# Kernel optimization log

Measured on AMD Instinct MI355X. Metric: run time of the kernel, lower is better.

The kernel has to match this reference:

```python
import jax, jax.numpy as jnp
import numpy as np

B, S, H = 2, 2048, 2048
NH, HD = 32, 64            # num heads, head dim (H = NH*HD)
FFN = 8192
EPS = 1e-5


def _layernorm(x, g, b):
    mu = jnp.mean(x, axis=-1, keepdims=True)
    var = jnp.mean(jnp.square(x - mu), axis=-1, keepdims=True)
    return (x - mu) * jax.lax.rsqrt(var + EPS) * g + b


def setup_inputs() -> dict:
    key = jax.random.key(0)
    ks = jax.random.split(key, 8)
    s = lambda fan_in: 1.0 / np.sqrt(fan_in)
    return {
        "x": jax.random.normal(ks[0], (B, S, H), dtype=jnp.float32),
        "ln1_g": jnp.ones((H,), jnp.float32),
        "ln1_b": jnp.zeros((H,), jnp.float32),
        "w_qkv": jax.random.normal(ks[1], (H, 3 * H), jnp.float32) * s(H),
        "b_qkv": jnp.zeros((3 * H,), jnp.float32),
        "w_proj": jax.random.normal(ks[2], (H, H), jnp.float32) * s(H),
        "b_proj": jnp.zeros((H,), jnp.float32),
        "ln2_g": jnp.ones((H,), jnp.float32),
        "ln2_b": jnp.zeros((H,), jnp.float32),
        "w1": jax.random.normal(ks[3], (H, FFN), jnp.float32) * s(H),
        "b1": jnp.zeros((FFN,), jnp.float32),
        "w2": jax.random.normal(ks[4], (FFN, H), jnp.float32) * s(FFN),
        "b2": jnp.zeros((H,), jnp.float32),
    }


def reference(x, ln1_g, ln1_b, w_qkv, b_qkv, w_proj, b_proj,
              ln2_g, ln2_b, w1, b1, w2, b2):
    # Pre-LN attention block (dropout in eval mode -> identity)
    res = x
    h = _layernorm(x, ln1_g, ln1_b)
    qkv = h @ w_qkv + b_qkv                       # [B,S,3H]
    qkv = qkv.reshape(B, S, NH, 3 * HD)           # matches tf reshape+split on axis 3
    q, k, v = jnp.split(qkv, 3, axis=3)           # each [B,S,NH,HD]
    scores = jnp.einsum('bqhd,bkhd->bhqk', q, k) / jnp.sqrt(jnp.float32(HD))
    probs = jax.nn.softmax(scores, axis=-1)       # [B,NH,S,S]
    ctx = jnp.einsum('bhqk,bkhd->bqhd', probs, v).reshape(B, S, H)
    x = ctx @ w_proj + b_proj
    x = res + x
    # Pre-LN MLP block
    res = x
    h = _layernorm(x, ln2_g, ln2_b)
    h = jax.nn.gelu(h @ w1 + b1, approximate=True)
    h = h @ w2 + b2
    return h + res
```

## Files before the change

### kernel.cpp

```cpp
#include <hip/hip_runtime.h>
#include <hip/hip_bf16.h>
#include <math.h>


typedef __attribute__((ext_vector_type(8))) short bf16x8;
typedef __attribute__((ext_vector_type(4))) float f32x4;
typedef __attribute__((ext_vector_type(16))) float f32x16;

#define DEV __device__ __forceinline__

static constexpr int SEQ  = 2048;
static constexpr int HID  = 2048;
static constexpr int NHEAD = 32;
static constexpr int HDIM = 64;
static constexpr int NFFN = 8192;
static constexpr int NTOK = 2 * SEQ;
static constexpr int QKVW = 3 * HID;

#define QSCALE 0.1803368801111204f

#if defined(__has_builtin)
#if __has_builtin(__builtin_amdgcn_exp2f)
#define EXP2(x) __builtin_amdgcn_exp2f(x)
#endif
#endif
#ifndef EXP2
#define EXP2(x) exp2f(x)
#endif

DEV ushort f2bf(float f) {
  unsigned u = __float_as_uint(f);
  return (ushort)((u + 0x7fffu + ((u >> 16) & 1u)) >> 16);
}

DEV void gload16(const void* g, void* l) {
  __builtin_amdgcn_global_load_lds(
      (const __attribute__((address_space(1))) unsigned int*)g,
      (__attribute__((address_space(3))) unsigned int*)l, 16, 0, 0);
}

__global__ __launch_bounds__(256) void tcvt_kernel(const float* __restrict__ in,
                                                   ushort* __restrict__ out,
                                                   int R, int C) {
  __shared__ ushort tile[64][72];
  const int tr = blockIdx.y * 64, tc = blockIdx.x * 64;
  const int t = threadIdx.x;
  const int rr = t >> 2, c4 = (t & 3) * 16;
  const float4* ip = (const float4*)(in + (size_t)(tr + rr) * C + tc + c4);
  float4 a0 = ip[0], a1 = ip[1], a2 = ip[2], a3 = ip[3];
  ushort* tp = &tile[rr][c4];
  tp[0]=f2bf(a0.x); tp[1]=f2bf(a0.y); tp[2]=f2bf(a0.z); tp[3]=f2bf(a0.w);
  tp[4]=f2bf(a1.x); tp[5]=f2bf(a1.y); tp[6]=f2bf(a1.z); tp[7]=f2bf(a1.w);
  tp[8]=f2bf(a2.x); tp[9]=f2bf(a2.y); tp[10]=f2bf(a2.z); tp[11]=f2bf(a2.w);
  tp[12]=f2bf(a3.x); tp[13]=f2bf(a3.y); tp[14]=f2bf(a3.z); tp[15]=f2bf(a3.w);
  __syncthreads();
  union { ushort u[8]; bf16x8 v; } p0, p1;
#pragma unroll
  for (int j = 0; j < 8; ++j) { p0.u[j] = tile[c4 + j][rr]; p1.u[j] = tile[c4 + 8 + j][rr]; }
  ushort* op = out + (size_t)(tc + rr) * R + tr + c4;
  *(bf16x8*)op = p0.v;
  *(bf16x8*)(op + 8) = p1.v;
}

__global__ __launch_bounds__(256) void ln_kernel(const float* __restrict__ x,
                                                 const float* __restrict__ g,
                                                 const float* __restrict__ bb,
                                                 ushort* __restrict__ out) {
  const int row = blockIdx.x, t = threadIdx.x;
  const float4* xv = (const float4*)(x + (size_t)row * HID);
  float4 a0 = xv[t * 2], a1 = xv[t * 2 + 1];
  float s  = a0.x + a0.y + a0.z + a0.w + a1.x + a1.y + a1.z + a1.w;
  float ss = a0.x*a0.x + a0.y*a0.y + a0.z*a0.z + a0.w*a0.w
           + a1.x*a1.x + a1.y*a1.y + a1.z*a1.z + a1.w*a1.w;
#pragma unroll
  for (int o = 32; o > 0; o >>= 1) { s += __shfl_down(s, o); ss += __shfl_down(ss, o); }
  __shared__ float red[8];
  const int w = t >> 6, l = t & 63;
  if (l == 0) { red[w] = s; red[4 + w] = ss; }
  __syncthreads();
  s  = red[0] + red[1] + red[2] + red[3];
  ss = red[4] + red[5] + red[6] + red[7];
  const float mu = s * (1.f / HID);
  const float rs = rsqrtf(ss * (1.f / HID) - mu * mu + 1e-5f);
  const float4* gv = (const float4*)g;
  const float4* bv = (const float4*)bb;
  float4 g0 = gv[t * 2], g1 = gv[t * 2 + 1], b0 = bv[t * 2], b1 = bv[t * 2 + 1];
  union { ushort u[8]; bf16x8 v; } p;
  p.u[0] = f2bf((a0.x - mu) * rs * g0.x + b0.x);
  p.u[1] = f2bf((a0.y - mu) * rs * g0.y + b0.y);
  p.u[2] = f2bf((a0.z - mu) * rs * g0.z + b0.z);
  p.u[3] = f2bf((a0.w - mu) * rs * g0.w + b0.w);
  p.u[4] = f2bf((a1.x - mu) * rs * g1.x + b1.x);
  p.u[5] = f2bf((a1.y - mu) * rs * g1.y + b1.y);
  p.u[6] = f2bf((a1.z - mu) * rs * g1.z + b1.z);
  p.u[7] = f2bf((a1.w - mu) * rs * g1.w + b1.w);
  *(bf16x8*)(out + (size_t)row * HID + t * 8) = p.v;
}

DEV void qkv_store(int row, int col, float v,
                   ushort* __restrict__ qpk, ushort* __restrict__ kpk,
                   ushort* __restrict__ vpk) {
  const int h = col / 192;
  const int c = col - h * 192;
  const int bh2 = (row >> 11) * 32 + h;
  const int t32 = (row >> 5) & 63;
  const int r5 = row & 31;
  if (c < 64) {
    const int s = c >> 4, hi2 = (c >> 3) & 1, j = c & 7;
    qpk[(((size_t)bh2 * 64 + t32) * 4 + s) * 512 + (hi2 * 32 + r5) * 8 + j] = f2bf(v * QSCALE);
  } else if (c < 128) {
    const int d = c - 64;
    const int s = d >> 4, hi2 = (d >> 3) & 1, j = d & 7;
    kpk[(((size_t)bh2 * 64 + t32) * 4 + s) * 512 + (hi2 * 32 + r5) * 8 + j] = f2bf(v);
  } else {
    const int d = c - 128;
    const int ks = r5 >> 4, hi2 = (r5 >> 3) & 1, j = r5 & 7;
    const int half = d >> 5, dl = d & 31;
    vpk[((((size_t)bh2 * 64 + t32) * 2 + ks) * 2 + half) * 512 + (hi2 * 32 + dl) * 8 + j] = f2bf(v);
  }
}

DEV bf16x8 ldsfrag(const char* base, int row, int slot) {
  return *(const bf16x8*)(base + row * 128 + (((slot ^ (row & 7)) << 4)));
}

DEV void stage_one(const ushort* __restrict__ src, int Kd, int trow, int kt,
                   char* dst, int w, int lr, int lsl, int i) {
  const int g = i * 8 + w;
  gload16(src + (size_t)(trow + g * 8 + lr) * Kd + kt + ((lsl ^ lr) << 3),
          dst + (g * 8 + lr) * 128 + lsl * 16);
}

template <int BM, int EPI>
__global__ __launch_bounds__(512, 2) void gemm8p_kernel(
    const ushort* __restrict__ A, const ushort* __restrict__ BT,
    const float* __restrict__ bias, const float* __restrict__ res,
    void* __restrict__ outv,
    ushort* __restrict__ qpk, ushort* __restrict__ kpk, ushort* __restrict__ vpk,
    int M, int N, int K) {
  constexpr int MR = BM / 32;
  constexpr int MH = MR / 2;
  constexpr int AI = BM / 64;
  constexpr int NI = AI + 4;
  constexpr int SPP = (BM == 256) ? 3 : 2;

  __shared__ ushort lds[2 * (BM * 64 + 256 * 64)];
  char* const a0p = (char*)lds;
  char* const b0p = a0p + BM * 128;
  char* const a1p = b0p + 32768;
  char* const b1p = a1p + BM * 128;

  const int t = threadIdx.x;
  const int w = t >> 6, l = t & 63;
  const int l16 = l & 15, lg = l >> 4;
  const int lr = l >> 3, lsl = l & 7;
  const int wm = w >> 2, wn = w & 3;

  const int nwg = gridDim.x * gridDim.y;
  const int lin = blockIdx.y * gridDim.x + blockIdx.x;
  const int work = (lin & 7) * (nwg >> 3) + (lin >> 3);
  const int bn = work % gridDim.x, bm = work / gridDim.x;
  const int tm = bm * BM, tn = bn * 256;

  const f32x4 z4 = {0.f, 0.f, 0.f, 0.f};
  f32x4 acc[MR][4];
#pragma unroll
  for (int i = 0; i < MR; ++i)
#pragma unroll
    for (int j = 0; j < 4; ++j) acc[i][j] = z4;

#pragma unroll
  for (int j = 0; j < NI; ++j) {
    if (j < 4) stage_one(BT, K, tn, 0, b0p, w, lr, lsl, j);
    else       stage_one(A,  K, tm, 0, a0p, w, lr, lsl, j - 4);
  }
  asm volatile("s_waitcnt vmcnt(0)" ::: "memory");
  __builtin_amdgcn_s_barrier();

#define KTILE(CA, CB, NA, NB, KTN, DOST)                                       \
  {                                                                            \
    _Pragma("unroll")                                                          \
    for (int q = 0; q < 4; ++q) {                                              \
      const int mh = q >> 1, nh = q & 1;                                       \
      bf16x8 af[MH][2], bfr[2][2];                                             \
      _Pragma("unroll")                                                        \
      for (int mi = 0; mi < MH; ++mi)                                          \
        _Pragma("unroll")                                                      \
        for (int ks = 0; ks < 2; ++ks)                                         \
          af[mi][ks] = ldsfrag(CA, wm * (BM / 2) + mh * (MH * 16) + mi * 16 + l16, ks * 4 + lg); \
      _Pragma("unroll")                                                        \
      for (int ni = 0; ni < 2; ++ni)                                           \
        _Pragma("unroll")                                                      \
        for (int ks = 0; ks < 2; ++ks)                                         \
          bfr[ni][ks] = ldsfrag(CB, wn * 64 + nh * 32 + ni * 16 + l16, ks * 4 + lg); \
      if (DOST) {                                                              \
        _Pragma("unroll")                                                      \
        for (int j = 0; j < SPP; ++j) {                                        \
          const int jj = q * SPP + j;                                          \
          if (jj < NI) {                                                       \
            if (jj < 4) stage_one(BT, K, tn, (KTN), NB, w, lr, lsl, jj);       \
            else        stage_one(A,  K, tm, (KTN), NA, w, lr, lsl, jj - 4);   \
          }                                                                    \
        }                                                                      \
      }                                                                        \
      __builtin_amdgcn_s_barrier();                                            \
      asm volatile("s_waitcnt lgkmcnt(0)" ::: "memory");                       \
      __builtin_amdgcn_sched_barrier(0);                                       \
      __builtin_amdgcn_s_setprio(1);                                           \
      _Pragma("unroll")                                                        \
      for (int mi = 0; mi < MH; ++mi)                                          \
        _Pragma("unroll")                                                      \
        for (int ni = 0; ni < 2; ++ni)                                         \
          _Pragma("unroll")                                                    \
          for (int ks = 0; ks < 2; ++ks)                                       \
            acc[mh * MH + mi][nh * 2 + ni] = __builtin_amdgcn_mfma_f32_16x16x32_bf16( \
                af[mi][ks], bfr[ni][ks], acc[mh * MH + mi][nh * 2 + ni], 0, 0, 0); \
      __builtin_amdgcn_s_setprio(0);                                           \
      if (q == 3 && (DOST)) asm volatile("s_waitcnt vmcnt(0)" ::: "memory");   \
      __builtin_amdgcn_s_barrier();                                            \
    }                                                                          \
  }

  const int nt = K >> 6;
  for (int it = 0; it < nt; it += 2) {
    KTILE(a0p, b0p, a1p, b1p, (it + 1) << 6, true);
    KTILE(a1p, b1p, a0p, b0p, (it + 2) << 6, (it + 2) < nt);
  }
#undef KTILE

  const int row0 = tm + wm * (BM / 2) + lg * 4;
  const int col0 = tn + wn * 64 + l16;
#pragma unroll
  for (int ni = 0; ni < 4; ++ni) {
    const int col = col0 + ni * 16;
    const float bvl = bias[col];
#pragma unroll
    for (int mi = 0; mi < MR; ++mi) {
#pragma unroll
      for (int r = 0; r < 4; ++r) {
        const int row = row0 + mi * 16 + r;
        float v = acc[mi][ni][r] + bvl;
        if (EPI == 1) {
          const size_t off = (size_t)row * N + col;
          ((float*)outv)[off] = v + res[off];
        } else if (EPI == 2) {
          const float u = 0.7978845608f * (v + 0.044715f * v * v * v);
          ((ushort*)outv)[(size_t)row * N + col] = f2bf(v / (1.f + __expf(-2.f * u)));
        } else if (EPI == 3) {
          qkv_store(row, col, v, qpk, kpk, vpk);
        } else {
          ((ushort*)outv)[(size_t)row * N + col] = f2bf(v);
        }
      }
    }
  }
}

__global__ __launch_bounds__(256) void attn_kernel(const ushort* __restrict__ qpk,
                                                   const ushort* __restrict__ kpk,
                                                   const ushort* __restrict__ vpk,
                                                   ushort* __restrict__ ctx) {
  const int lin = blockIdx.x + blockIdx.y * gridDim.x;
  const int work = (lin & 7) * 128 + (lin >> 3);
  const int qt = work & 15, bh = work >> 4;
  const int b = bh >> 5, h = bh & 31;
  const int t = threadIdx.x, w = t >> 6, l = t & 63;
  const int l32 = l & 31, hi = l >> 5;

  const ushort* qb = qpk + ((((size_t)bh * 64 + qt * 4 + w) * 4) * 64 + l) * 8;
  bf16x8 qf0 = *(const bf16x8*)(qb);
  bf16x8 qf1 = *(const bf16x8*)(qb + 512);
  bf16x8 qf2 = *(const bf16x8*)(qb + 1024);
  bf16x8 qf3 = *(const bf16x8*)(qb + 1536);

  const ushort* kbase = kpk + (size_t)bh * 131072 + l * 8;
  const ushort* vbase = vpk + (size_t)bh * 131072 + l * 8;

  f32x16 oacc0, oacc1;
#pragma unroll
  for (int r = 0; r < 16; ++r) { oacc0[r] = 0.f; oacc1[r] = 0.f; }
  float m = -1e30f, lsum = 0.f;
  const f32x16 z16 = {};

#define LOADK(k0, k1, k2, k3, kt) {                                           \
    const ushort* p_ = kbase + (size_t)(kt) * 2048;                           \
    k0 = *(const bf16x8*)(p_);        k1 = *(const bf16x8*)(p_ + 512);        \
    k2 = *(const bf16x8*)(p_ + 1024); k3 = *(const bf16x8*)(p_ + 1536); }
#define LOADV(v0, v1, v2, v3, kt) {                                           \
    const ushort* p_ = vbase + (size_t)(kt) * 2048;                           \
    v0 = *(const bf16x8*)(p_);        v1 = *(const bf16x8*)(p_ + 512);        \
    v2 = *(const bf16x8*)(p_ + 1024); v3 = *(const bf16x8*)(p_ + 1536); }

#define STEP(k0, k1, k2, k3, v0, v1, v2, v3) {                                \
    f32x16 s = __builtin_amdgcn_mfma_f32_32x32x16_bf16(k0, qf0, z16, 0, 0, 0);\
    s = __builtin_amdgcn_mfma_f32_32x32x16_bf16(k1, qf1, s, 0, 0, 0);         \
    s = __builtin_amdgcn_mfma_f32_32x32x16_bf16(k2, qf2, s, 0, 0, 0);         \
    s = __builtin_amdgcn_mfma_f32_32x32x16_bf16(k3, qf3, s, 0, 0, 0);         \
    float tm = s[0];                                                          \
    _Pragma("unroll") for (int r = 1; r < 16; ++r) tm = fmaxf(tm, s[r]);      \
    tm = fmaxf(tm, __shfl_xor(tm, 32));                                       \
    if (!__all(tm - m <= 8.f)) {                                              \
      const float mn = fmaxf(m, tm);                                          \
      const float sf = EXP2(m - mn);                                          \
      m = mn;                                                                 \
      lsum *= sf;                                                             \
      _Pragma("unroll") for (int r = 0; r < 16; ++r) {                        \
        const float f = __shfl(sf, (r & 3) + 8 * (r >> 2) + 4 * hi);          \
        oacc0[r] *= f; oacc1[r] *= f;                                         \
      }                                                                       \
    }                                                                         \
    float p[16];                                                              \
    _Pragma("unroll") for (int r = 0; r < 16; ++r) p[r] = EXP2(s[r] - m);     \
    float ls = 0.f;                                                           \
    _Pragma("unroll") for (int r = 0; r < 16; ++r) ls += p[r];                \
    lsum += ls;                                                               \
    unsigned pw[8];                                                           \
    _Pragma("unroll") for (int i = 0; i < 8; ++i)                             \
      asm("v_cvt_pk_bf16_f32 %0, %1, %2" : "=v"(pw[i]) : "v"(p[2*i]), "v"(p[2*i+1])); \
    unsigned a0 = pw[0], b0 = pw[2];                                          \
    asm("v_permlane32_swap_b32 %0, %1" : "+v"(a0), "+v"(b0));                 \
    unsigned a1 = pw[1], b1 = pw[3];                                          \
    asm("v_permlane32_swap_b32 %0, %1" : "+v"(a1), "+v"(b1));                 \
    unsigned a2 = pw[4], b2 = pw[6];                                          \
    asm("v_permlane32_swap_b32 %0, %1" : "+v"(a2), "+v"(b2));                 \
    unsigned a3 = pw[5], b3 = pw[7];                                          \
    asm("v_permlane32_swap_b32 %0, %1" : "+v"(a3), "+v"(b3));                 \
    union { unsigned uw[4]; bf16x8 v; } pa0, pa1;                             \
    pa0.uw[0] = a0; pa0.uw[1] = a1; pa0.uw[2] = b0; pa0.uw[3] = b1;           \
    pa1.uw[0] = a2; pa1.uw[1] = a3; pa1.uw[2] = b2; pa1.uw[3] = b3;           \
    oacc0 = __builtin_amdgcn_mfma_f32_32x32x16_bf16(pa0.v, v0, oacc0, 0, 0, 0);\
    oacc1 = __builtin_amdgcn_mfma_f32_32x32x16_bf16(pa0.v, v1, oacc1, 0, 0, 0);\
    oacc0 = __builtin_amdgcn_mfma_f32_32x32x16_bf16(pa1.v, v2, oacc0, 0, 0, 0);\
    oacc1 = __builtin_amdgcn_mfma_f32_32x32x16_bf16(pa1.v, v3, oacc1, 0, 0, 0);}

  bf16x8 ka0, ka1, ka2, ka3, kc0, kc1, kc2, kc3;
  LOADK(ka0, ka1, ka2, ka3, 0);
  for (int kt = 0; kt < 64; kt += 2) {
    bf16x8 va0, va1, va2, va3;
    LOADV(va0, va1, va2, va3, kt);
    LOADK(kc0, kc1, kc2, kc3, kt + 1);
    STEP(ka0, ka1, ka2, ka3, va0, va1, va2, va3);
    LOADV(va0, va1, va2, va3, kt + 1);
    if (kt + 2 < 64) LOADK(ka0, ka1, ka2, ka3, kt + 2);
    STEP(kc0, kc1, kc2, kc3, va0, va1, va2, va3);
  }
#undef LOADK
#undef LOADV
#undef STEP

  const float lf = lsum + __shfl_xor(lsum, 32);
  const float linv = 1.f / lf;
#pragma unroll
  for (int r = 0; r < 16; ++r) {
    const int qr = (r & 3) + 8 * (r >> 2);
    const float fac = __shfl(linv, qr + 4 * hi);
    const int row = qt * 128 + w * 32 + qr + 4 * hi;
    const size_t base = ((size_t)(b * SEQ + row)) * HID + h * 64 + l32;
    ctx[base]      = f2bf(oacc0[r] * fac);
    ctx[base + 32] = f2bf(oacc1[r] * fac);
  }
}

extern "C" void kernel_launch(void* const* d_in, const int* in_sizes, int n_in,
                              void* d_out, int out_size, void* d_ws, size_t ws_size,
                              hipStream_t stream) {
  const float* x      = (const float*)d_in[0];
  const float* ln1g   = (const float*)d_in[1];
  const float* ln1b   = (const float*)d_in[2];
  const float* w_qkv  = (const float*)d_in[3];
  const float* b_qkv  = (const float*)d_in[4];
  const float* w_proj = (const float*)d_in[5];
  const float* b_proj = (const float*)d_in[6];
  const float* ln2g   = (const float*)d_in[7];
  const float* ln2b   = (const float*)d_in[8];
  const float* w1     = (const float*)d_in[9];
  const float* b1     = (const float*)d_in[10];
  const float* w2     = (const float*)d_in[11];
  const float* b2     = (const float*)d_in[12];

  char* ws = (char*)d_ws;
  ushort* wqkvT  = (ushort*)(ws + 0);
  ushort* wprojT = (ushort*)(ws + 25165824);
  ushort* w1T    = (ushort*)(ws + 33554432);
  ushort* w2T    = (ushort*)(ws + 67108864);
  ushort* hbuf   = (ushort*)(ws + 100663296);
  ushort* qpk    = (ushort*)(ws + 117440512);
  ushort* kpk    = (ushort*)(ws + 134217728);
  ushort* vpk    = (ushort*)(ws + 150994944);
  ushort* ctxb   = (ushort*)(ws + 167772160);
  ushort* gelu   = (ushort*)(ws + 117440512);
  float*  x2     = (float*)(ws + 184549376);

  tcvt_kernel<<<dim3(96, 32),  256, 0, stream>>>(w_qkv,  wqkvT, 2048, 6144);
  tcvt_kernel<<<dim3(32, 32),  256, 0, stream>>>(w_proj, wprojT, 2048, 2048);
  tcvt_kernel<<<dim3(128, 32), 256, 0, stream>>>(w1,     w1T,   2048, 8192);
  tcvt_kernel<<<dim3(32, 128), 256, 0, stream>>>(w2,     w2T,   8192, 2048);

  ln_kernel<<<NTOK, 256, 0, stream>>>(x, ln1g, ln1b, hbuf);
  gemm8p_kernel<128, 3><<<dim3(24, 32), 512, 0, stream>>>(
      hbuf, wqkvT, b_qkv, nullptr, nullptr, qpk, kpk, vpk, NTOK, QKVW, HID);
  attn_kernel<<<dim3(16, 2 * NHEAD), 256, 0, stream>>>(qpk, kpk, vpk, ctxb);
  gemm8p_kernel<128, 1><<<dim3(8, 32), 512, 0, stream>>>(
      ctxb, wprojT, b_proj, x, x2, nullptr, nullptr, nullptr, NTOK, HID, HID);
  ln_kernel<<<NTOK, 256, 0, stream>>>(x2, ln2g, ln2b, hbuf);
  gemm8p_kernel<256, 2><<<dim3(32, 16), 512, 0, stream>>>(
      hbuf, w1T, b1, nullptr, gelu, nullptr, nullptr, nullptr, NTOK, NFFN, HID);
  gemm8p_kernel<128, 1><<<dim3(8, 32), 512, 0, stream>>>(
      gelu, w2T, b2, x2, (float*)d_out, nullptr, nullptr, nullptr, NTOK, HID, NFFN);
}
```

Baseline: 748.4 us.

## Reorder GEMM LDS staging by quadrant with partial vmcnt waits and fewer barriers

```diff
diff --git a/kernel.cpp b/kernel.cpp
--- a/kernel.cpp
+++ b/kernel.cpp
@@ -27,6 +27,8 @@
 #ifndef EXP2
 #define EXP2(x) exp2f(x)
 #endif
+
+#define VMCNT(n) asm volatile("s_waitcnt vmcnt(" #n ")" ::: "memory")
 
 DEV ushort f2bf(float f) {
   unsigned u = __float_as_uint(f);
@@ -124,11 +126,78 @@
   return *(const bf16x8*)(base + row * 128 + (((slot ^ (row & 7)) << 4)));
 }
 
-DEV void stage_one(const ushort* __restrict__ src, int Kd, int trow, int kt,
-                   char* dst, int w, int lr, int lsl, int i) {
-  const int g = i * 8 + w;
-  gload16(src + (size_t)(trow + g * 8 + lr) * Kd + kt + ((lsl ^ lr) << 3),
-          dst + (g * 8 + lr) * 128 + lsl * 16);
+template <int BM>
+DEV void stageA(const ushort* __restrict__ A, int Kd, int tm, int kt,
+                char* abuf, int w, int lr, int lsl, int mh, int s) {
+  int row;
+  if (BM == 256) {
+    row = s * 128 + mh * 64 + w * 8 + lr;
+  } else {
+    const int ri = w * 8 + lr;
+    row = (ri >> 5) * 64 + mh * 32 + (ri & 31);
+  }
+  gload16(A + (size_t)(tm + row) * Kd + kt + ((lsl ^ lr) << 3),
+          abuf + row * 128 + lsl * 16);
+}
+
+DEV void stageB(const ushort* __restrict__ BT, int Kd, int tn, int kt,
+                char* bbuf, int w, int lr, int lsl, int nh, int s) {
+  const int ri = s * 64 + w * 8 + lr;
+  const int row = (ri >> 5) * 64 + nh * 32 + (ri & 31);
+  gload16(BT + (size_t)(tn + row) * Kd + kt + ((lsl ^ lr) << 3),
+          bbuf + row * 128 + lsl * 16);
+}
+
+template <int BM>
+DEV void ktile(const ushort* __restrict__ A, const ushort* __restrict__ BT,
+               int K, int tm, int tn,
+               const char* CA, const char* CB, char* NA, char* NB,
+               int ktn, bool dost, int w, int l, f32x4 (&acc)[BM / 32][4]) {
+  constexpr int MH = BM / 64;
+  const int l16 = l & 15, lg = l >> 4, lr = l >> 3, lsl = l & 7;
+  const int wm = w >> 2, wn = w & 3;
+  bf16x8 af[MH][2];
+#pragma unroll
+  for (int q = 0; q < 4; ++q) {
+    const int mh = q >> 1, nh = q & 1;
+    if ((q & 1) == 0) {
+#pragma unroll
+      for (int mi = 0; mi < MH; ++mi)
+#pragma unroll
+        for (int ks = 0; ks < 2; ++ks)
+          af[mi][ks] = ldsfrag(CA, wm * (BM / 2) + mh * (BM / 4) + mi * 16 + l16, ks * 4 + lg);
+    }
+    bf16x8 bfr[2][2];
+#pragma unroll
+    for (int ni = 0; ni < 2; ++ni)
+#pragma unroll
+      for (int ks = 0; ks < 2; ++ks)
+        bfr[ni][ks] = ldsfrag(CB, wn * 64 + nh * 32 + ni * 16 + l16, ks * 4 + lg);
+    if (dost && q < 2) {
+      stageA<BM>(A, K, tm, ktn, NA, w, lr, lsl, q, 0);
+      if (BM == 256) stageA<BM>(A, K, tm, ktn, NA, w, lr, lsl, q, 1);
+      stageB(BT, K, tn, ktn, NB, w, lr, lsl, q, 0);
+      stageB(BT, K, tn, ktn, NB, w, lr, lsl, q, 1);
+    }
+    if (q == 0) {
+      if (dost) { if (BM == 256) VMCNT(4); else VMCNT(3); }
+      else VMCNT(0);
+    }
+    if (q == 3 && dost) { if (BM == 256) VMCNT(4); else VMCNT(3); }
+    __builtin_amdgcn_s_barrier();
+    asm volatile("s_waitcnt lgkmcnt(0)" ::: "memory");
+    __builtin_amdgcn_sched_barrier(0);
+    __builtin_amdgcn_s_setprio(1);
+#pragma unroll
+    for (int mi = 0; mi < MH; ++mi)
+#pragma unroll
+      for (int ni = 0; ni < 2; ++ni)
+#pragma unroll
+        for (int ks = 0; ks < 2; ++ks)
+          acc[mh * MH + mi][nh * 2 + ni] = __builtin_amdgcn_mfma_f32_16x16x32_bf16(
+              af[mi][ks], bfr[ni][ks], acc[mh * MH + mi][nh * 2 + ni], 0, 0, 0);
+    __builtin_amdgcn_s_setprio(0);
+  }
 }
 
 template <int BM, int EPI>
@@ -139,10 +208,6 @@
     ushort* __restrict__ qpk, ushort* __restrict__ kpk, ushort* __restrict__ vpk,
     int M, int N, int K) {
   constexpr int MR = BM / 32;
-  constexpr int MH = MR / 2;
-  constexpr int AI = BM / 64;
-  constexpr int NI = AI + 4;
-  constexpr int SPP = (BM == 256) ? 3 : 2;
 
   __shared__ ushort lds[2 * (BM * 64 + 256 * 64)];
   char* const a0p = (char*)lds;
@@ -170,63 +235,20 @@
     for (int j = 0; j < 4; ++j) acc[i][j] = z4;
 
 #pragma unroll
-  for (int j = 0; j < NI; ++j) {
-    if (j < 4) stage_one(BT, K, tn, 0, b0p, w, lr, lsl, j);
-    else       stage_one(A,  K, tm, 0, a0p, w, lr, lsl, j - 4);
-  }
-  asm volatile("s_waitcnt vmcnt(0)" ::: "memory");
+  for (int mh = 0; mh < 2; ++mh) {
+    stageA<BM>(A, K, tm, 0, a0p, w, lr, lsl, mh, 0);
+    if (BM == 256) stageA<BM>(A, K, tm, 0, a0p, w, lr, lsl, mh, 1);
+    stageB(BT, K, tn, 0, b0p, w, lr, lsl, mh, 0);
+    stageB(BT, K, tn, 0, b0p, w, lr, lsl, mh, 1);
+  }
+  VMCNT(0);
   __builtin_amdgcn_s_barrier();
-
-#define KTILE(CA, CB, NA, NB, KTN, DOST)                                       \
-  {                                                                            \
-    _Pragma("unroll")                                                          \
-    for (int q = 0; q < 4; ++q) {                                              \
-      const int mh = q >> 1, nh = q & 1;                                       \
-      bf16x8 af[MH][2], bfr[2][2];                                             \
-      _Pragma("unroll")                                                        \
-      for (int mi = 0; mi < MH; ++mi)                                          \
-        _Pragma("unroll")                                                      \
-        for (int ks = 0; ks < 2; ++ks)                                         \
-          af[mi][ks] = ldsfrag(CA, wm * (BM / 2) + mh * (MH * 16) + mi * 16 + l16, ks * 4 + lg); \
-      _Pragma("unroll")                                                        \
-      for (int ni = 0; ni < 2; ++ni)                                           \
-        _Pragma("unroll")                                                      \
-        for (int ks = 0; ks < 2; ++ks)                                         \
-          bfr[ni][ks] = ldsfrag(CB, wn * 64 + nh * 32 + ni * 16 + l16, ks * 4 + lg); \
-      if (DOST) {                                                              \
-        _Pragma("unroll")                                                      \
-        for (int j = 0; j < SPP; ++j) {                                        \
-          const int jj = q * SPP + j;                                          \
-          if (jj < NI) {                                                       \
-            if (jj < 4) stage_one(BT, K, tn, (KTN), NB, w, lr, lsl, jj);       \
-            else        stage_one(A,  K, tm, (KTN), NA, w, lr, lsl, jj - 4);   \
-          }                                                                    \
-        }                                                                      \
-      }                                                                        \
-      __builtin_amdgcn_s_barrier();                                            \
-      asm volatile("s_waitcnt lgkmcnt(0)" ::: "memory");                       \
-      __builtin_amdgcn_sched_barrier(0);                                       \
-      __builtin_amdgcn_s_setprio(1);                                           \
-      _Pragma("unroll")                                                        \
-      for (int mi = 0; mi < MH; ++mi)                                          \
-        _Pragma("unroll")                                                      \
-        for (int ni = 0; ni < 2; ++ni)                                         \
-          _Pragma("unroll")                                                    \
-          for (int ks = 0; ks < 2; ++ks)                                       \
-            acc[mh * MH + mi][nh * 2 + ni] = __builtin_amdgcn_mfma_f32_16x16x32_bf16( \
-                af[mi][ks], bfr[ni][ks], acc[mh * MH + mi][nh * 2 + ni], 0, 0, 0); \
-      __builtin_amdgcn_s_setprio(0);                                           \
-      if (q == 3 && (DOST)) asm volatile("s_waitcnt vmcnt(0)" ::: "memory");   \
-      __builtin_amdgcn_s_barrier();                                            \
-    }                                                                          \
-  }
 
   const int nt = K >> 6;
   for (int it = 0; it < nt; it += 2) {
-    KTILE(a0p, b0p, a1p, b1p, (it + 1) << 6, true);
-    KTILE(a1p, b1p, a0p, b0p, (it + 2) << 6, (it + 2) < nt);
-  }
-#undef KTILE
+    ktile<BM>(A, BT, K, tm, tn, a0p, b0p, a1p, b1p, (it + 1) << 6, true, w, l, acc);
+    ktile<BM>(A, BT, K, tm, tn, a1p, b1p, a0p, b0p, (it + 2) << 6, (it + 2) < nt, w, l, acc);
+  }
 
   const int row0 = tm + wm * (BM / 2) + lg * 4;
   const int col0 = tn + wn * 64 + l16;
@@ -296,11 +318,11 @@
     s = __builtin_amdgcn_mfma_f32_32x32x16_bf16(k1, qf1, s, 0, 0, 0);         \
     s = __builtin_amdgcn_mfma_f32_32x32x16_bf16(k2, qf2, s, 0, 0, 0);         \
     s = __builtin_amdgcn_mfma_f32_32x32x16_bf16(k3, qf3, s, 0, 0, 0);         \
-    float tm = s[0];                                                          \
-    _Pragma("unroll") for (int r = 1; r < 16; ++r) tm = fmaxf(tm, s[r]);      \
-    tm = fmaxf(tm, __shfl_xor(tm, 32));                                       \
-    if (!__all(tm - m <= 8.f)) {                                              \
-      const float mn = fmaxf(m, tm);                                          \
+    float tm_ = s[0];                                                         \
+    _Pragma("unroll") for (int r = 1; r < 16; ++r) tm_ = fmaxf(tm_, s[r]);    \
+    tm_ = fmaxf(tm_, __shfl_xor(tm_, 32));                                    \
+    if (!__all(tm_ - m <= 8.f)) {                                             \
+      const float mn = fmaxf(m, tm_);                                         \
       const float sf = EXP2(m - mn);                                          \
       m = mn;                                                                 \
       lsum *= sf;                                                             \
```

After: 633.9 us. -15.3%, faster.
